# Kernel tuning notes

Hardware: AMD Instinct MI355X
Metric: run time of the kernel (lower is better)

Reference implementation:

```python
import jax, jax.numpy as jnp
import numpy as np

N_LAYERS = 3
N_NODES = 512
D_IN = 4  # dimensions + 1
BATCH = 131072


def _glorot(key, shape):
    fan_in, fan_out = shape[-2], shape[-1]
    lim = np.sqrt(6.0 / (fan_in + fan_out))
    return jax.random.uniform(key, shape, jnp.float32, -lim, lim)


def setup_inputs() -> dict:
    key = jax.random.key(0)
    ks = jax.random.split(key, 12)
    L, n, d = N_LAYERS, N_NODES, D_IN
    return {
        "X": jax.random.normal(ks[0], (BATCH, d), jnp.float32),
        "W_in": _glorot(ks[1], (d, n)),
        "b_in": jnp.zeros((1, n), jnp.float32),
        "Wf": _glorot(ks[2], (L, d, n)),
        "Uf": _glorot(ks[3], (L, n, n)),
        "bf": jnp.zeros((L, 1, n), jnp.float32),
        "Wu": _glorot(ks[4], (L, d, n)),
        "Uu": _glorot(ks[5], (L, n, n)),
        "bu": jnp.zeros((L, 1, n), jnp.float32),
        "Wo1": _glorot(ks[6], (L, d, n)),
        "Uo1": _glorot(ks[7], (L, n, n)),
        "bo1": jnp.zeros((L, 1, n), jnp.float32),
        "Wo2": _glorot(ks[8], (L, n, n)),
        "bo2": jnp.zeros((L, 1, n), jnp.float32),
        "W_out": _glorot(ks[9], (n, 1)),
        "b_out": jnp.zeros((1, 1), jnp.float32),
    }


def reference(X, W_in, b_in, Wf, Uf, bf, Wu, Uu, bu, Wo1, Uo1, bo1, Wo2, bo2, W_out, b_out):
    # initial dense layer with swish activation
    H = jax.nn.silu(X @ W_in + b_in)  # [B, n_nodes]
    for i in range(N_LAYERS):
        F = jax.nn.sigmoid(X @ Wf[i] + H @ Uf[i] + bf[i])
        U = jax.nn.sigmoid(X @ Wu[i] + H @ Uu[i] + bu[i])
        O1 = jnp.tanh(X @ Wo1[i] + H @ Uo1[i] + bo1[i])
        O2 = jax.nn.silu((U * O1) @ Wo2[i] + bo2[i])
        H = F * H + O2
    return jax.nn.silu(H @ W_out + b_out)  # [B, 1]
```

## Files before the change

### kernel.cpp

```cpp
#include <hip/hip_runtime.h>
#include <cstdint>
#include <cstddef>

#define NLAYERS 3
#define NN      512
#define DIN     4
#define MTILE   64
#define KAUG    544
#define LDA     552
#define WELEMS  (NN * KAUG)
#define LDS_BYTES (2 * MTILE * LDA * 2)
#define NTHREADS 512

typedef __attribute__((ext_vector_type(8))) short short8;
typedef __attribute__((ext_vector_type(4))) float f32x4;

__device__ __forceinline__ short f2bf(float f) {
    union { float f; uint32_t u; } v; v.f = f;
    uint32_t r = v.u + 0x7fffu + ((v.u >> 16) & 1u);
    return (short)(r >> 16);
}
__device__ __forceinline__ float bf2f(short s) {
    union { uint32_t u; float f; } v; v.u = ((uint32_t)(uint16_t)s) << 16;
    return v.f;
}
__device__ __forceinline__ float sig_(float x)  { return 1.0f / (1.0f + __expf(-x)); }
__device__ __forceinline__ float tanh_(float x) { return 1.0f - 2.0f / (1.0f + __expf(2.0f * x)); }
__device__ __forceinline__ float silu_(float x) { return x / (1.0f + __expf(-x)); }

__global__ void prep_kernel(const float* __restrict__ Wf,  const float* __restrict__ Uf,  const float* __restrict__ bf,
                            const float* __restrict__ Wu,  const float* __restrict__ Uu,  const float* __restrict__ bu,
                            const float* __restrict__ Wo1, const float* __restrict__ Uo1, const float* __restrict__ bo1,
                            const float* __restrict__ Wo2, const float* __restrict__ bo2,
                            short* __restrict__ ws) {
    int idx = blockIdx.x * 256 + threadIdx.x;
    int m   = idx / WELEMS;
    if (m >= 12) return;
    int rem = idx - m * WELEMS;
    int n   = rem / KAUG;
    int kk  = rem - n * KAUG;
    int layer = m >> 2, t = m & 3;
    const float* U; const float* W; const float* b;
    switch (t) {
        case 0:  U = Uf;  W = Wf;      b = bf;  break;
        case 1:  U = Uu;  W = Wu;      b = bu;  break;
        case 2:  U = Uo1; W = Wo1;     b = bo1; break;
        default: U = Wo2; W = nullptr; b = bo2; break;
    }
    float val = 0.0f;
    if (kk < NN)             val = U[layer * NN * NN + kk * NN + n];
    else if (kk < NN + DIN)  val = W ? W[layer * DIN * NN + (kk - NN) * NN + n] : 0.0f;
    else if (kk == NN + DIN) val = b[layer * NN + n];
    ws[idx] = f2bf(val);
}

struct Frag { short8 v[4]; };

__device__ __forceinline__ void loadA(Frag& f, const short* a, int k) {
#pragma unroll
    for (int i = 0; i < 4; ++i) f.v[i] = *(const short8*)(a + i * 16 * LDA + k);
}
__device__ __forceinline__ void loadB(Frag& f, const short* b, int k) {
#pragma unroll
    for (int i = 0; i < 4; ++i) f.v[i] = *(const short8*)(b + i * 16 * KAUG + k);
}
__device__ __forceinline__ void mf16(f32x4 (&acc)[4][4], const Frag& A, const Frag& B) {
#pragma unroll
    for (int mt = 0; mt < 4; ++mt)
#pragma unroll
        for (int nt = 0; nt < 4; ++nt)
            acc[mt][nt] = __builtin_amdgcn_mfma_f32_16x16x32_bf16(A.v[mt], B.v[nt], acc[mt][nt], 0, 0, 0);
}

__device__ __forceinline__ void mm1(const short* __restrict__ Asrc, const short* __restrict__ Bt,
                                    int n0, int l16, int quad, f32x4 (&acc)[4][4]) {
#pragma unroll
    for (int mt = 0; mt < 4; ++mt)
#pragma unroll
        for (int nt = 0; nt < 4; ++nt) acc[mt][nt] = f32x4{0.f, 0.f, 0.f, 0.f};
    const short* a0 = Asrc + l16 * LDA + quad * 8;
    const short* b0 = Bt + (size_t)(n0 + l16) * KAUG + quad * 8;
    Frag aA, bA, aB, bB;
    loadA(aA, a0, 0); loadB(bA, b0, 0);
#pragma unroll 1
    for (int i = 0; i < 8; ++i) {
        const int k = i * 64;
        loadA(aB, a0, k + 32); loadB(bB, b0, k + 32);
        mf16(acc, aA, bA);
        loadA(aA, a0, k + 64); loadB(bA, b0, k + 64);
        mf16(acc, aB, bB);
    }
    mf16(acc, aA, bA);
}

__global__ void __launch_bounds__(NTHREADS, 2)
dgm_kernel(const float* __restrict__ X, const float* __restrict__ W_in, const float* __restrict__ b_in,
           const float* __restrict__ W_out, const float* __restrict__ b_out,
           const short* __restrict__ wmats, float* __restrict__ out) {
    extern __shared__ short lds[];
    short* Hb = lds;
    short* Tb = lds + MTILE * LDA;

    const int tid  = threadIdx.x;
    const int lane = tid & 63;
    const int wv   = tid >> 6;
    const int l16  = lane & 15;
    const int quad = lane >> 4;
    const int n0   = wv * 64;
    const int rbase = blockIdx.x * MTILE;

#pragma unroll 4
    for (int j = 0; j < (MTILE * NN) / NTHREADS; ++j) {
        int idx = tid + j * NTHREADS;
        int r = idx >> 9;
        int c = idx & (NN - 1);
        const float* xr = X + (size_t)(rbase + r) * DIN;
        float v = b_in[c];
#pragma unroll
        for (int k = 0; k < DIN; ++k) v += xr[k] * W_in[k * NN + c];
        Hb[r * LDA + c] = f2bf(silu_(v));
    }
    if (tid < MTILE) {
        int r = tid;
        const float* xr = X + (size_t)(rbase + r) * DIN;
#pragma unroll
        for (int k = 0; k < DIN; ++k) {
            Hb[r * LDA + NN + k] = f2bf(xr[k]);
            Tb[r * LDA + NN + k] = 0;
        }
        Hb[r * LDA + NN + DIN] = f2bf(1.0f);
        Tb[r * LDA + NN + DIN] = f2bf(1.0f);
        for (int k = NN + DIN + 1; k < KAUG; ++k) {
            Hb[r * LDA + k] = 0;
            Tb[r * LDA + k] = 0;
        }
    }
    __syncthreads();

    uint32_t Fpack[32];

    for (int layer = 0; layer < NLAYERS; ++layer) {
        const short* wF  = wmats + (size_t)(layer * 4 + 0) * WELEMS;
        const short* wU  = wmats + (size_t)(layer * 4 + 1) * WELEMS;
        const short* wO1 = wmats + (size_t)(layer * 4 + 2) * WELEMS;
        const short* wO2 = wmats + (size_t)(layer * 4 + 3) * WELEMS;

        uint32_t Tpack[32];
        {
            f32x4 aO[4][4];
            mm1(Hb, wO1, n0, l16, quad, aO);
#pragma unroll
            for (int mt = 0; mt < 4; ++mt)
#pragma unroll
                for (int nt = 0; nt < 4; ++nt)
#pragma unroll
                    for (int rp = 0; rp < 2; ++rp) {
                        uint32_t lo = (uint16_t)f2bf(tanh_(aO[mt][nt][2 * rp + 0]));
                        uint32_t hi = (uint16_t)f2bf(tanh_(aO[mt][nt][2 * rp + 1]));
                        Tpack[mt * 8 + nt * 2 + rp] = lo | (hi << 16);
                    }
        }
        {
            f32x4 aU[4][4];
            mm1(Hb, wU, n0, l16, quad, aU);
#pragma unroll
            for (int mt = 0; mt < 4; ++mt)
#pragma unroll
                for (int nt = 0; nt < 4; ++nt)
#pragma unroll
                    for (int rg = 0; rg < 4; ++rg) {
                        uint32_t tp = Tpack[mt * 8 + nt * 2 + (rg >> 1)];
                        float to = bf2f((short)(uint16_t)((rg & 1) ? (tp >> 16) : (tp & 0xffffu)));
                        int row = mt * 16 + quad * 4 + rg;
                        int col = n0 + nt * 16 + l16;
                        Tb[row * LDA + col] = f2bf(sig_(aU[mt][nt][rg]) * to);
                    }
        }
        {
            f32x4 aF[4][4];
            mm1(Hb, wF, n0, l16, quad, aF);
#pragma unroll
            for (int mt = 0; mt < 4; ++mt)
#pragma unroll
                for (int nt = 0; nt < 4; ++nt)
#pragma unroll
                    for (int rp = 0; rp < 2; ++rp) {
                        uint32_t lo = (uint16_t)f2bf(sig_(aF[mt][nt][2 * rp + 0]));
                        uint32_t hi = (uint16_t)f2bf(sig_(aF[mt][nt][2 * rp + 1]));
                        Fpack[mt * 8 + nt * 2 + rp] = lo | (hi << 16);
                    }
        }
        __syncthreads();

        {
            f32x4 aO2[4][4];
            mm1(Tb, wO2, n0, l16, quad, aO2);
#pragma unroll
            for (int mt = 0; mt < 4; ++mt)
#pragma unroll
                for (int nt = 0; nt < 4; ++nt)
#pragma unroll
                    for (int rg = 0; rg < 4; ++rg) {
                        uint32_t fp = Fpack[mt * 8 + nt * 2 + (rg >> 1)];
                        float f = bf2f((short)(uint16_t)((rg & 1) ? (fp >> 16) : (fp & 0xffffu)));
                        int row = mt * 16 + quad * 4 + rg;
                        int col = n0 + nt * 16 + l16;
                        float hold = bf2f(Hb[row * LDA + col]);
                        float o2 = silu_(aO2[mt][nt][rg]);
                        Hb[row * LDA + col] = f2bf(f * hold + o2);
                    }
        }
        __syncthreads();
    }

    {
        const int r = tid >> 3, q = tid & 7;
        const int c0 = q * (NN / 8);
        float p = 0.0f;
        for (int c = c0; c < c0 + NN / 8; ++c)
            p += bf2f(Hb[r * LDA + c]) * W_out[c];
        float* red = (float*)Tb;
        red[tid] = p;
        __syncthreads();
        if (q == 0) {
            float s = b_out[0];
#pragma unroll
            for (int i = 0; i < 8; ++i) s += red[r * 8 + i];
            out[rbase + r] = silu_(s);
        }
    }
}

extern "C" void kernel_launch(void* const* d_in, const int* in_sizes, int n_in,
                              void* d_out, int out_size, void* d_ws, size_t ws_size,
                              hipStream_t stream) {
    const float* X     = (const float*)d_in[0];
    const float* W_in  = (const float*)d_in[1];
    const float* b_in  = (const float*)d_in[2];
    const float* Wf    = (const float*)d_in[3];
    const float* Uf    = (const float*)d_in[4];
    const float* bf    = (const float*)d_in[5];
    const float* Wu    = (const float*)d_in[6];
    const float* Uu    = (const float*)d_in[7];
    const float* bu    = (const float*)d_in[8];
    const float* Wo1   = (const float*)d_in[9];
    const float* Uo1   = (const float*)d_in[10];
    const float* bo1   = (const float*)d_in[11];
    const float* Wo2   = (const float*)d_in[12];
    const float* bo2   = (const float*)d_in[13];
    const float* W_out = (const float*)d_in[14];
    const float* b_out = (const float*)d_in[15];
    float* out = (float*)d_out;
    short* ws  = (short*)d_ws;

    const int B = in_sizes[0] / DIN;

    prep_kernel<<<(12 * WELEMS + 255) / 256, 256, 0, stream>>>(
        Wf, Uf, bf, Wu, Uu, bu, Wo1, Uo1, bo1, Wo2, bo2, ws);

    hipFuncSetAttribute((const void*)dgm_kernel,
                        hipFuncAttributeMaxDynamicSharedMemorySize, LDS_BYTES);
    dgm_kernel<<<B / MTILE, NTHREADS, LDS_BYTES, stream>>>(X, W_in, b_in, W_out, b_out, ws, out);
}
```

Baseline: 1.419 ms.

## Double threads per block, halve per-wave N tile to 32 columns

Block size goes from 512 to 1024 threads (16 waves), and each wave now computes a 64x32 output tile instead of 64x64. Accumulators, packed F/T registers and B-fragment loads are halved, and launch bounds ask for 4 blocks per CU. The aim is lower register pressure and more waves in flight to hide LDS and global latency. In exchange each wave re-reads the same A fragments from LDS for half as much MFMA work, so LDS traffic per FLOP doubles, and LDS size may still cap residency.

```diff
diff --git a/kernel.cpp b/kernel.cpp
--- a/kernel.cpp
+++ b/kernel.cpp
@@ -10,7 +10,7 @@
 #define LDA     552
 #define WELEMS  (NN * KAUG)
 #define LDS_BYTES (2 * MTILE * LDA * 2)
-#define NTHREADS 512
+#define NTHREADS 1024
 
 typedef __attribute__((ext_vector_type(8))) short short8;
 typedef __attribute__((ext_vector_type(4))) float f32x4;
@@ -54,46 +54,51 @@
     ws[idx] = f2bf(val);
 }
 
-struct Frag { short8 v[4]; };
-
-__device__ __forceinline__ void loadA(Frag& f, const short* a, int k) {
-#pragma unroll
-    for (int i = 0; i < 4; ++i) f.v[i] = *(const short8*)(a + i * 16 * LDA + k);
-}
-__device__ __forceinline__ void loadB(Frag& f, const short* b, int k) {
-#pragma unroll
-    for (int i = 0; i < 4; ++i) f.v[i] = *(const short8*)(b + i * 16 * KAUG + k);
-}
-__device__ __forceinline__ void mf16(f32x4 (&acc)[4][4], const Frag& A, const Frag& B) {
+__device__ __forceinline__ void mm1(const short* __restrict__ Asrc, const short* __restrict__ Bt,
+                                    int n0, int l16, int quad, f32x4 (&acc)[4][2]) {
 #pragma unroll
     for (int mt = 0; mt < 4; ++mt)
 #pragma unroll
-        for (int nt = 0; nt < 4; ++nt)
-            acc[mt][nt] = __builtin_amdgcn_mfma_f32_16x16x32_bf16(A.v[mt], B.v[nt], acc[mt][nt], 0, 0, 0);
-}
-
-__device__ __forceinline__ void mm1(const short* __restrict__ Asrc, const short* __restrict__ Bt,
-                                    int n0, int l16, int quad, f32x4 (&acc)[4][4]) {
-#pragma unroll
-    for (int mt = 0; mt < 4; ++mt)
-#pragma unroll
-        for (int nt = 0; nt < 4; ++nt) acc[mt][nt] = f32x4{0.f, 0.f, 0.f, 0.f};
-    const short* a0 = Asrc + l16 * LDA + quad * 8;
-    const short* b0 = Bt + (size_t)(n0 + l16) * KAUG + quad * 8;
-    Frag aA, bA, aB, bB;
-    loadA(aA, a0, 0); loadB(bA, b0, 0);
+        for (int nt = 0; nt < 2; ++nt) acc[mt][nt] = f32x4{0.f, 0.f, 0.f, 0.f};
+    const short* aP = Asrc + l16 * LDA + quad * 8;
+    const short* bP = Bt + (size_t)(n0 + l16) * KAUG + quad * 8;
+
+    short8 aA[4], bA[2], aB[4], bB[2];
+#pragma unroll
+    for (int mt = 0; mt < 4; ++mt) aA[mt] = *(const short8*)(aP + mt * 16 * LDA);
+    bA[0] = *(const short8*)(bP);
+    bA[1] = *(const short8*)(bP + 16 * KAUG);
+
 #pragma unroll 1
     for (int i = 0; i < 8; ++i) {
-        const int k = i * 64;
-        loadA(aB, a0, k + 32); loadB(bB, b0, k + 32);
-        mf16(acc, aA, bA);
-        loadA(aA, a0, k + 64); loadB(bA, b0, k + 64);
-        mf16(acc, aB, bB);
-    }
-    mf16(acc, aA, bA);
-}
-
-__global__ void __launch_bounds__(NTHREADS, 2)
+#pragma unroll
+        for (int mt = 0; mt < 4; ++mt) aB[mt] = *(const short8*)(aP + mt * 16 * LDA + 32);
+        bB[0] = *(const short8*)(bP + 32);
+        bB[1] = *(const short8*)(bP + 16 * KAUG + 32);
+#pragma unroll
+        for (int mt = 0; mt < 4; ++mt) {
+            acc[mt][0] = __builtin_amdgcn_mfma_f32_16x16x32_bf16(aA[mt], bA[0], acc[mt][0], 0, 0, 0);
+            acc[mt][1] = __builtin_amdgcn_mfma_f32_16x16x32_bf16(aA[mt], bA[1], acc[mt][1], 0, 0, 0);
+        }
+#pragma unroll
+        for (int mt = 0; mt < 4; ++mt) aA[mt] = *(const short8*)(aP + mt * 16 * LDA + 64);
+        bA[0] = *(const short8*)(bP + 64);
+        bA[1] = *(const short8*)(bP + 16 * KAUG + 64);
+#pragma unroll
+        for (int mt = 0; mt < 4; ++mt) {
+            acc[mt][0] = __builtin_amdgcn_mfma_f32_16x16x32_bf16(aB[mt], bB[0], acc[mt][0], 0, 0, 0);
+            acc[mt][1] = __builtin_amdgcn_mfma_f32_16x16x32_bf16(aB[mt], bB[1], acc[mt][1], 0, 0, 0);
+        }
+        aP += 64; bP += 64;
+    }
+#pragma unroll
+    for (int mt = 0; mt < 4; ++mt) {
+        acc[mt][0] = __builtin_amdgcn_mfma_f32_16x16x32_bf16(aA[mt], bA[0], acc[mt][0], 0, 0, 0);
+        acc[mt][1] = __builtin_amdgcn_mfma_f32_16x16x32_bf16(aA[mt], bA[1], acc[mt][1], 0, 0, 0);
+    }
+}
+
+__global__ void __launch_bounds__(NTHREADS, 4)
 dgm_kernel(const float* __restrict__ X, const float* __restrict__ W_in, const float* __restrict__ b_in,
            const float* __restrict__ W_out, const float* __restrict__ b_out,
            const short* __restrict__ wmats, float* __restrict__ out) {
@@ -106,7 +111,7 @@
     const int wv   = tid >> 6;
     const int l16  = lane & 15;
     const int quad = lane >> 4;
-    const int n0   = wv * 64;
+    const int n0   = wv * 32;
     const int rbase = blockIdx.x * MTILE;
 
 #pragma unroll 4
@@ -137,7 +142,7 @@
     }
     __syncthreads();
 
-    uint32_t Fpack[32];
+    uint32_t Fpack[16];
 
     for (int layer = 0; layer < NLAYERS; ++layer) {
         const short* wF  = wmats + (size_t)(layer * 4 + 0) * WELEMS;
@@ -145,31 +150,31 @@
         const short* wO1 = wmats + (size_t)(layer * 4 + 2) * WELEMS;
         const short* wO2 = wmats + (size_t)(layer * 4 + 3) * WELEMS;
 
-        uint32_t Tpack[32];
-        {
-            f32x4 aO[4][4];
+        uint32_t Tpack[16];
+        {
+            f32x4 aO[4][2];
             mm1(Hb, wO1, n0, l16, quad, aO);
 #pragma unroll
             for (int mt = 0; mt < 4; ++mt)
 #pragma unroll
-                for (int nt = 0; nt < 4; ++nt)
+                for (int nt = 0; nt < 2; ++nt)
 #pragma unroll
                     for (int rp = 0; rp < 2; ++rp) {
                         uint32_t lo = (uint16_t)f2bf(tanh_(aO[mt][nt][2 * rp + 0]));
                         uint32_t hi = (uint16_t)f2bf(tanh_(aO[mt][nt][2 * rp + 1]));
-                        Tpack[mt * 8 + nt * 2 + rp] = lo | (hi << 16);
-                    }
-        }
-        {
-            f32x4 aU[4][4];
+                        Tpack[mt * 4 + nt * 2 + rp] = lo | (hi << 16);
+                    }
+        }
+        {
+            f32x4 aU[4][2];
             mm1(Hb, wU, n0, l16, quad, aU);
 #pragma unroll
             for (int mt = 0; mt < 4; ++mt)
 #pragma unroll
-                for (int nt = 0; nt < 4; ++nt)
+                for (int nt = 0; nt < 2; ++nt)
 #pragma unroll
                     for (int rg = 0; rg < 4; ++rg) {
-                        uint32_t tp = Tpack[mt * 8 + nt * 2 + (rg >> 1)];
+                        uint32_t tp = Tpack[mt * 4 + nt * 2 + (rg >> 1)];
                         float to = bf2f((short)(uint16_t)((rg & 1) ? (tp >> 16) : (tp & 0xffffu)));
                         int row = mt * 16 + quad * 4 + rg;
                         int col = n0 + nt * 16 + l16;
@@ -177,31 +182,31 @@
                     }
         }
         {
-            f32x4 aF[4][4];
+            f32x4 aF[4][2];
             mm1(Hb, wF, n0, l16, quad, aF);
 #pragma unroll
             for (int mt = 0; mt < 4; ++mt)
 #pragma unroll
-                for (int nt = 0; nt < 4; ++nt)
+                for (int nt = 0; nt < 2; ++nt)
 #pragma unroll
                     for (int rp = 0; rp < 2; ++rp) {
                         uint32_t lo = (uint16_t)f2bf(sig_(aF[mt][nt][2 * rp + 0]));
                         uint32_t hi = (uint16_t)f2bf(sig_(aF[mt][nt][2 * rp + 1]));
-                        Fpack[mt * 8 + nt * 2 + rp] = lo | (hi << 16);
+                        Fpack[mt * 4 + nt * 2 + rp] = lo | (hi << 16);
                     }
         }
         __syncthreads();
 
         {
-            f32x4 aO2[4][4];
+            f32x4 aO2[4][2];
             mm1(Tb, wO2, n0, l16, quad, aO2);
 #pragma unroll
             for (int mt = 0; mt < 4; ++mt)
 #pragma unroll
-                for (int nt = 0; nt < 4; ++nt)
+                for (int nt = 0; nt < 2; ++nt)
 #pragma unroll
                     for (int rg = 0; rg < 4; ++rg) {
-                        uint32_t fp = Fpack[mt * 8 + nt * 2 + (rg >> 1)];
+                        uint32_t fp = Fpack[mt * 4 + nt * 2 + (rg >> 1)];
                         float f = bf2f((short)(uint16_t)((rg & 1) ? (fp >> 16) : (fp & 0xffffu)));
                         int row = mt * 16 + quad * 4 + rg;
                         int col = n0 + nt * 16 + l16;
@@ -214,10 +219,10 @@
     }
 
     {
-        const int r = tid >> 3, q = tid & 7;
-        const int c0 = q * (NN / 8);
+        const int r = tid >> 4, q = tid & 15;
+        const int c0 = q * (NN / 16);
         float p = 0.0f;
-        for (int c = c0; c < c0 + NN / 8; ++c)
+        for (int c = c0; c < c0 + NN / 16; ++c)
             p += bf2f(Hb[r * LDA + c]) * W_out[c];
         float* red = (float*)Tb;
         red[tid] = p;
@@ -225,7 +230,7 @@
         if (q == 0) {
             float s = b_out[0];
 #pragma unroll
-            for (int i = 0; i < 8; ++i) s += red[r * 8 + i];
+            for (int i = 0; i < 16; ++i) s += red[r * 16 + i];
             out[rbase + r] = silu_(s);
         }
     }
```

After: 1.335 ms. 1.06x faster.

## Fuse F/U/O1 GEMMs into one pass sharing A fragments with interleaved weights

Applied to the files above, without the earlier changes.

Reorders the prepared bf16 weights so the F, U and O1 matrices for each output column are interleaved, and computes all three gates in a single K loop that loads each LDS A fragment once and feeds three MFMA accumulator sets. This cuts LDS A reads by a factor of three, removes the Tpack bf16 round trip for O1, and computes U*O1 directly in fp32. The cost is three 4x4 accumulator arrays plus double-buffered B fragments held live at once, which raises register pressure under launch_bounds(512,2) and may cause spills or lower occupancy. The wave index is also made scalar with readfirstlane.

```diff
diff --git a/kernel.cpp b/kernel.cpp
--- a/kernel.cpp
+++ b/kernel.cpp
@@ -34,12 +34,23 @@
                             const float* __restrict__ Wo2, const float* __restrict__ bo2,
                             short* __restrict__ ws) {
     int idx = blockIdx.x * 256 + threadIdx.x;
-    int m   = idx / WELEMS;
-    if (m >= 12) return;
-    int rem = idx - m * WELEMS;
-    int n   = rem / KAUG;
-    int kk  = rem - n * KAUG;
-    int layer = m >> 2, t = m & 3;
+    if (idx >= 12 * WELEMS) return;
+    int layer, t, n, kk;
+    if (idx < 9 * WELEMS) {
+        layer   = idx / (3 * WELEMS);
+        int rem = idx - layer * 3 * WELEMS;
+        n       = rem / (3 * KAUG);
+        int r2  = rem - n * 3 * KAUG;
+        t       = r2 / KAUG;
+        kk      = r2 - t * KAUG;
+    } else {
+        int i2  = idx - 9 * WELEMS;
+        layer   = i2 / WELEMS;
+        int rem = i2 - layer * WELEMS;
+        n       = rem / KAUG;
+        kk      = rem - n * KAUG;
+        t       = 3;
+    }
     const float* U; const float* W; const float* b;
     switch (t) {
         case 0:  U = Uf;  W = Wf;      b = bf;  break;
@@ -54,22 +65,66 @@
     ws[idx] = f2bf(val);
 }
 
-struct Frag { short8 v[4]; };
-
-__device__ __forceinline__ void loadA(Frag& f, const short* a, int k) {
-#pragma unroll
-    for (int i = 0; i < 4; ++i) f.v[i] = *(const short8*)(a + i * 16 * LDA + k);
-}
-__device__ __forceinline__ void loadB(Frag& f, const short* b, int k) {
-#pragma unroll
-    for (int i = 0; i < 4; ++i) f.v[i] = *(const short8*)(b + i * 16 * KAUG + k);
-}
-__device__ __forceinline__ void mf16(f32x4 (&acc)[4][4], const Frag& A, const Frag& B) {
+__device__ __forceinline__ void mm3(const short* __restrict__ Asrc, const short* __restrict__ fused,
+                                    int n0, int l16, int quad,
+                                    f32x4 (&aF)[4][4], f32x4 (&aU)[4][4], f32x4 (&aO)[4][4]) {
 #pragma unroll
     for (int mt = 0; mt < 4; ++mt)
 #pragma unroll
-        for (int nt = 0; nt < 4; ++nt)
-            acc[mt][nt] = __builtin_amdgcn_mfma_f32_16x16x32_bf16(A.v[mt], B.v[nt], acc[mt][nt], 0, 0, 0);
+        for (int nt = 0; nt < 4; ++nt) {
+            aF[mt][nt] = f32x4{0.f, 0.f, 0.f, 0.f};
+            aU[mt][nt] = f32x4{0.f, 0.f, 0.f, 0.f};
+            aO[mt][nt] = f32x4{0.f, 0.f, 0.f, 0.f};
+        }
+    const short* aP = Asrc + l16 * LDA + quad * 8;
+    const short* p0 = fused + (size_t)(n0 +  0 + l16) * 3 * KAUG + quad * 8;
+    const short* p1 = fused + (size_t)(n0 + 16 + l16) * 3 * KAUG + quad * 8;
+    const short* p2 = fused + (size_t)(n0 + 32 + l16) * 3 * KAUG + quad * 8;
+    const short* p3 = fused + (size_t)(n0 + 48 + l16) * 3 * KAUG + quad * 8;
+
+    short8 avA[4], avB[4];
+    short8 bFA[4], bUA[4], bOA[4], bFB[4], bUB[4], bOB[4];
+
+#define LD_A(dst, off) { \
+    dst[0] = *(const short8*)(aP + 0 * 16 * LDA + (off)); \
+    dst[1] = *(const short8*)(aP + 1 * 16 * LDA + (off)); \
+    dst[2] = *(const short8*)(aP + 2 * 16 * LDA + (off)); \
+    dst[3] = *(const short8*)(aP + 3 * 16 * LDA + (off)); }
+#define LD_B(dF, dU, dO, off) { \
+    dF[0] = *(const short8*)(p0 + (off));             dU[0] = *(const short8*)(p0 + KAUG + (off)); \
+    dO[0] = *(const short8*)(p0 + 2 * KAUG + (off)); \
+    dF[1] = *(const short8*)(p1 + (off));             dU[1] = *(const short8*)(p1 + KAUG + (off)); \
+    dO[1] = *(const short8*)(p1 + 2 * KAUG + (off)); \
+    dF[2] = *(const short8*)(p2 + (off));             dU[2] = *(const short8*)(p2 + KAUG + (off)); \
+    dO[2] = *(const short8*)(p2 + 2 * KAUG + (off)); \
+    dF[3] = *(const short8*)(p3 + (off));             dU[3] = *(const short8*)(p3 + KAUG + (off)); \
+    dO[3] = *(const short8*)(p3 + 2 * KAUG + (off)); }
+#define MFMA3(av, bF, bU, bO) { \
+    _Pragma("unroll") \
+    for (int mt = 0; mt < 4; ++mt) { \
+        _Pragma("unroll") \
+        for (int nt = 0; nt < 4; ++nt) { \
+            aF[mt][nt] = __builtin_amdgcn_mfma_f32_16x16x32_bf16(av[mt], bF[nt], aF[mt][nt], 0, 0, 0); \
+            aU[mt][nt] = __builtin_amdgcn_mfma_f32_16x16x32_bf16(av[mt], bU[nt], aU[mt][nt], 0, 0, 0); \
+            aO[mt][nt] = __builtin_amdgcn_mfma_f32_16x16x32_bf16(av[mt], bO[nt], aO[mt][nt], 0, 0, 0); \
+        } } }
+
+    LD_A(avA, 0);
+    LD_B(bFA, bUA, bOA, 0);
+#pragma unroll 1
+    for (int i = 0; i < 8; ++i) {
+        LD_A(avB, 32);
+        LD_B(bFB, bUB, bOB, 32);
+        MFMA3(avA, bFA, bUA, bOA);
+        LD_A(avA, 64);
+        LD_B(bFA, bUA, bOA, 64);
+        MFMA3(avB, bFB, bUB, bOB);
+        aP += 64; p0 += 64; p1 += 64; p2 += 64; p3 += 64;
+    }
+    MFMA3(avA, bFA, bUA, bOA);
+#undef LD_A
+#undef LD_B
+#undef MFMA3
 }
 
 __device__ __forceinline__ void mm1(const short* __restrict__ Asrc, const short* __restrict__ Bt,
@@ -78,19 +133,39 @@
     for (int mt = 0; mt < 4; ++mt)
 #pragma unroll
         for (int nt = 0; nt < 4; ++nt) acc[mt][nt] = f32x4{0.f, 0.f, 0.f, 0.f};
-    const short* a0 = Asrc + l16 * LDA + quad * 8;
-    const short* b0 = Bt + (size_t)(n0 + l16) * KAUG + quad * 8;
-    Frag aA, bA, aB, bB;
-    loadA(aA, a0, 0); loadB(bA, b0, 0);
+    const short* aP = Asrc + l16 * LDA + quad * 8;
+    const short* q0 = Bt + (size_t)(n0 +  0 + l16) * KAUG + quad * 8;
+    const short* q1 = Bt + (size_t)(n0 + 16 + l16) * KAUG + quad * 8;
+    const short* q2 = Bt + (size_t)(n0 + 32 + l16) * KAUG + quad * 8;
+    const short* q3 = Bt + (size_t)(n0 + 48 + l16) * KAUG + quad * 8;
+    short8 aA[4], bA[4], aB[4], bB[4];
+#define LD_A1(dst, off) { \
+    dst[0] = *(const short8*)(aP + 0 * 16 * LDA + (off)); \
+    dst[1] = *(const short8*)(aP + 1 * 16 * LDA + (off)); \
+    dst[2] = *(const short8*)(aP + 2 * 16 * LDA + (off)); \
+    dst[3] = *(const short8*)(aP + 3 * 16 * LDA + (off)); }
+#define LD_B1(dst, off) { \
+    dst[0] = *(const short8*)(q0 + (off)); dst[1] = *(const short8*)(q1 + (off)); \
+    dst[2] = *(const short8*)(q2 + (off)); dst[3] = *(const short8*)(q3 + (off)); }
+#define MFMA1(av, bv) { \
+    _Pragma("unroll") \
+    for (int mt = 0; mt < 4; ++mt) { \
+        _Pragma("unroll") \
+        for (int nt = 0; nt < 4; ++nt) \
+            acc[mt][nt] = __builtin_amdgcn_mfma_f32_16x16x32_bf16(av[mt], bv[nt], acc[mt][nt], 0, 0, 0); } }
+    LD_A1(aA, 0); LD_B1(bA, 0);
 #pragma unroll 1
     for (int i = 0; i < 8; ++i) {
-        const int k = i * 64;
-        loadA(aB, a0, k + 32); loadB(bB, b0, k + 32);
-        mf16(acc, aA, bA);
-        loadA(aA, a0, k + 64); loadB(bA, b0, k + 64);
-        mf16(acc, aB, bB);
-    }
-    mf16(acc, aA, bA);
+        LD_A1(aB, 32); LD_B1(bB, 32);
+        MFMA1(aA, bA);
+        LD_A1(aA, 64); LD_B1(bA, 64);
+        MFMA1(aB, bB);
+        aP += 64; q0 += 64; q1 += 64; q2 += 64; q3 += 64;
+    }
+    MFMA1(aA, bA);
+#undef LD_A1
+#undef LD_B1
+#undef MFMA1
 }
 
 __global__ void __launch_bounds__(NTHREADS, 2)
@@ -103,7 +178,7 @@
 
     const int tid  = threadIdx.x;
     const int lane = tid & 63;
-    const int wv   = tid >> 6;
+    const int wv   = __builtin_amdgcn_readfirstlane(tid >> 6);
     const int l16  = lane & 15;
     const int quad = lane >> 4;
     const int n0   = wv * 64;
@@ -140,45 +215,24 @@
     uint32_t Fpack[32];
 
     for (int layer = 0; layer < NLAYERS; ++layer) {
-        const short* wF  = wmats + (size_t)(layer * 4 + 0) * WELEMS;
-        const short* wU  = wmats + (size_t)(layer * 4 + 1) * WELEMS;
-        const short* wO1 = wmats + (size_t)(layer * 4 + 2) * WELEMS;
-        const short* wO2 = wmats + (size_t)(layer * 4 + 3) * WELEMS;
-
-        uint32_t Tpack[32];
+        const short* wFUO = wmats + (size_t)layer * 3 * WELEMS;
+        const short* wO2  = wmats + (size_t)9 * WELEMS + (size_t)layer * WELEMS;
+
         {
-            f32x4 aO[4][4];
-            mm1(Hb, wO1, n0, l16, quad, aO);
+            f32x4 aF[4][4], aU[4][4], aO[4][4];
+            mm3(Hb, wFUO, n0, l16, quad, aF, aU, aO);
 #pragma unroll
             for (int mt = 0; mt < 4; ++mt)
 #pragma unroll
                 for (int nt = 0; nt < 4; ++nt)
 #pragma unroll
-                    for (int rp = 0; rp < 2; ++rp) {
-                        uint32_t lo = (uint16_t)f2bf(tanh_(aO[mt][nt][2 * rp + 0]));
-                        uint32_t hi = (uint16_t)f2bf(tanh_(aO[mt][nt][2 * rp + 1]));
-                        Tpack[mt * 8 + nt * 2 + rp] = lo | (hi << 16);
-                    }
-        }
-        {
-            f32x4 aU[4][4];
-            mm1(Hb, wU, n0, l16, quad, aU);
-#pragma unroll
-            for (int mt = 0; mt < 4; ++mt)
-#pragma unroll
-                for (int nt = 0; nt < 4; ++nt)
-#pragma unroll
                     for (int rg = 0; rg < 4; ++rg) {
-                        uint32_t tp = Tpack[mt * 8 + nt * 2 + (rg >> 1)];
-                        float to = bf2f((short)(uint16_t)((rg & 1) ? (tp >> 16) : (tp & 0xffffu)));
                         int row = mt * 16 + quad * 4 + rg;
                         int col = n0 + nt * 16 + l16;
-                        Tb[row * LDA + col] = f2bf(sig_(aU[mt][nt][rg]) * to);
+                        float uu = sig_(aU[mt][nt][rg]);
+                        float oo = tanh_(aO[mt][nt][rg]);
+                        Tb[row * LDA + col] = f2bf(uu * oo);
                     }
-        }
-        {
-            f32x4 aF[4][4];
-            mm1(Hb, wF, n0, l16, quad, aF);
 #pragma unroll
             for (int mt = 0; mt < 4; ++mt)
 #pragma unroll
```

New measurement: 1.975 ms. 1.39x slower.
